# Kernel tuning notes

Measured on AMD Instinct MI355X. Metric: run time of the kernel, lower is better.

The kernel has to match this reference:

```python
import jax, jax.numpy as jnp
import numpy as np

N = 50000          # number of points
C = 64             # num_clusters (embedding width)
K_RAD = 32         # radius graph max_num_neighbors
K_KNN = 10         # knn graph k


def setup_inputs() -> dict:
    key = jax.random.key(0)
    ks = jax.random.split(key, 8)
    x0 = jax.random.normal(ks[0], (N, 3), jnp.float32)
    pos0 = jax.random.normal(ks[1], (N, 3), jnp.float32)
    # R0/t0 come from rigid_fitting in the original (external helper); use
    # orthonormal matrices from batched QR as realistic per-point rotations.
    A = jax.random.normal(ks[2], (N, 3, 3), jnp.float32)
    R0, _ = jnp.linalg.qr(A)
    t0 = jax.random.normal(ks[3], (N, 3), jnp.float32) * 0.1
    # pool1 k=1 assignment: point i -> cluster assign01[i]
    assign01 = jax.random.randint(ks[4], (N,), 0, C, dtype=jnp.int32)
    # radius graph edges (source, target): each point has K_RAD neighbors
    radius_src = jax.random.randint(ks[5], (N * K_RAD,), 0, N, dtype=jnp.int32)
    radius_dst = jnp.repeat(jnp.arange(N, dtype=jnp.int32), K_RAD)
    # knn-10 graph edges used by WeightedAvg
    knn_src = jax.random.randint(ks[6], (N * K_KNN,), 0, N, dtype=jnp.int32)
    knn_dst = jnp.repeat(jnp.arange(N, dtype=jnp.int32), K_KNN)
    return dict(x0=x0, pos0=pos0, R0=R0, t0=t0, assign01=assign01,
                radius_src=radius_src, radius_dst=radius_dst,
                knn_src=knn_src, knn_dst=knn_dst)


def _rigid_layer(xfeat, pos0, x0, R0, t0, src, dst):
    # RigidPropModule.message + max aggregation (nn=None, lin1: w=-1, b=0.01)
    Ri = R0[dst]                     # [E,3,3] target-side rotation
    ti = t0[dst]                     # [E,3]
    posj = pos0[src]                 # [E,3]
    xj = x0[src]                     # [E,3]
    pred = jnp.einsum('eij,ej->ei', Ri, posj) + ti
    d = jnp.sum((pred - xj) ** 2, axis=-1, keepdims=True)   # [E,1]
    w = jax.nn.sigmoid(-d + 0.01)
    msg = w * xfeat[src]             # [E,C]
    agg = jax.ops.segment_max(msg, dst, num_segments=xfeat.shape[0])
    # messages are non-negative; nodes with no edges get 0 (torch_scatter fill)
    return jnp.maximum(agg, 0.0)


def reference(x0, pos0, R0, t0, assign01, radius_src, radius_dst, knn_src, knn_dst):
    n = x0.shape[0]
    # scatter_add of one-hot cluster embeddings back to points
    emb = jnp.zeros((n, C), jnp.float32).at[jnp.arange(n), assign01].add(1.0)
    m1 = _rigid_layer(emb, pos0, x0, R0, t0, radius_src, radius_dst)
    m2 = _rigid_layer(m1, pos0, x0, R0, t0, radius_src, radius_dst)
    m3 = _rigid_layer(m2, pos0, x0, R0, t0, radius_src, radius_dst)
    m4 = _rigid_layer(m2, pos0, x0, R0, t0, radius_src, radius_dst)
    m5 = _rigid_layer(m2, pos0, x0, R0, t0, radius_src, radius_dst)
    msg = jnp.stack([m1.sum(-1), m2.sum(-1), m3.sum(-1),
                     m4.sum(-1), m5.sum(-1)], axis=-1)      # [N,5]
    # predictor: Linear(5,1) with w=ones, b=-17, then sigmoid
    conf = jax.nn.sigmoid(msg.sum(-1, keepdims=True) - 17.0)  # [N,1]
    # WeightedAvg over knn edges: out[t] = sum_s conf[s]*val[s] / sum_s conf[s]
    cw = conf[knn_src]                                       # [E,1]
    num_R = jax.ops.segment_sum(cw * R0.reshape(n, 9)[knn_src], knn_dst, num_segments=n)
    num_t = jax.ops.segment_sum(cw * t0[knn_src], knn_dst, num_segments=n)
    den = jax.ops.segment_sum(cw, knn_dst, num_segments=n) + 1e-8
    R_out = (num_R / den).reshape(n, 3, 3)
    t_out = num_t / den
    x_out = jnp.einsum('nij,nj->ni', R_out, pos0) + t_out
    return x_out, R_out, t_out
```

## Files before the change

kernel.cpp:

```cpp
#include <hip/hip_runtime.h>
#include <hip/hip_fp16.h>
#include <math.h>

#define N_PTS 50000
#define C_DIM 64
#define K_RAD 32
#define K_KNN 10

typedef unsigned int uv4 __attribute__((ext_vector_type(4)));
typedef unsigned int uv2 __attribute__((ext_vector_type(2)));

__device__ inline __half2 hmax2(__half2 a, __half2 b) {
    __half2 d;
    asm("v_pk_max_f16 %0, %1, %2" : "=v"(d) : "v"(a), "v"(b));
    return d;
}

__device__ inline __half2 shfl_xor_h2(__half2 v, int mask) {
    int i = *(int*)&v;
    int r = __shfl_xor(i, mask);
    return *(__half2*)&r;
}

__global__ void pack_tables_kernel(const float* __restrict__ pos0,
                                   const float* __restrict__ x0,
                                   const int* __restrict__ assign,
                                   float4* __restrict__ geo) {
    int i = blockIdx.x * blockDim.x + threadIdx.x;
    if (i >= N_PTS) return;
    geo[i * 2 + 0] = make_float4(pos0[3 * i], pos0[3 * i + 1], pos0[3 * i + 2], x0[3 * i]);
    geo[i * 2 + 1] = make_float4(x0[3 * i + 1], x0[3 * i + 2], __int_as_float(assign[i]), 0.0f);
}

__global__ void ew_layer1_kernel(const float4* __restrict__ geo,
                                 const float* __restrict__ R0,
                                 const float* __restrict__ t0,
                                 const int* __restrict__ src,
                                 unsigned int* __restrict__ packed,
                                 __half* __restrict__ m1,
                                 float4* __restrict__ rt4) {
    __shared__ int lm[16][C_DIM];
    __shared__ float ldsR[16 * 9];
    __shared__ float ldsT[16 * 3];
    float* rt4f = (float*)rt4;
    int tid = threadIdx.x;
    int blk = blockIdx.x;
    ((int*)lm)[tid] = 0;
    ((int*)lm)[tid + 256] = 0;
    ((int*)lm)[tid + 512] = 0;
    ((int*)lm)[tid + 768] = 0;
    if (tid < 144) ldsR[tid] = R0[blk * 144 + tid];
    if (tid < 48) ldsT[tid] = t0[blk * 48 + tid];
    int nl = tid >> 4;
    int ng = blk * 16 + nl;
    int e0 = tid & 15, e1 = e0 + 16;
    int s0 = __builtin_nontemporal_load(src + ng * K_RAD + e0);
    int s1 = __builtin_nontemporal_load(src + ng * K_RAD + e1);
    float4 g0a = geo[s0 * 2 + 0];
    float4 g0b = geo[s0 * 2 + 1];
    float4 g1a = geo[s1 * 2 + 0];
    float4 g1b = geo[s1 * 2 + 1];
    __syncthreads();
    if (tid < 48) {
        int n = tid / 3, slot = tid % 3;
        const float* Rp = ldsR + n * 9;
        const float* Tp = ldsT + n * 3;
        float4 q;
        if (slot == 0) q = make_float4(Rp[0], Rp[1], Rp[2], Rp[3]);
        else if (slot == 1) q = make_float4(Rp[4], Rp[5], Rp[6], Rp[7]);
        else q = make_float4(Rp[8], Tp[0], Tp[1], Tp[2]);
        rt4[(blk * 16 + n) * 4 + slot] = q;
    }
    const float* R = ldsR + nl * 9;
    const float* T = ldsT + nl * 3;
    float r0 = R[0] * g0a.x + R[1] * g0a.y + R[2] * g0a.z + T[0] - g0a.w;
    float r1 = R[3] * g0a.x + R[4] * g0a.y + R[5] * g0a.z + T[1] - g0b.x;
    float r2 = R[6] * g0a.x + R[7] * g0a.y + R[8] * g0a.z + T[2] - g0b.y;
    float d0 = r0 * r0 + r1 * r1 + r2 * r2;
    float w0 = 1.0f / (1.0f + __expf(d0 - 0.01f));
    float u0 = R[0] * g1a.x + R[1] * g1a.y + R[2] * g1a.z + T[0] - g1a.w;
    float u1 = R[3] * g1a.x + R[4] * g1a.y + R[5] * g1a.z + T[1] - g1b.x;
    float u2 = R[6] * g1a.x + R[7] * g1a.y + R[8] * g1a.z + T[2] - g1b.y;
    float d1 = u0 * u0 + u1 * u1 + u2 * u2;
    float w1 = 1.0f / (1.0f + __expf(d1 - 0.01f));
    unsigned int p0 =
        ((unsigned int)s0 << 16) | (unsigned int)__half_as_ushort(__float2half_rn(w0));
    unsigned int p1 =
        ((unsigned int)s1 << 16) | (unsigned int)__half_as_ushort(__float2half_rn(w1));
    __builtin_nontemporal_store(p0, packed + ng * K_RAD + e0);
    __builtin_nontemporal_store(p1, packed + ng * K_RAD + e1);
    atomicMax(&lm[nl][__float_as_int(g0b.z)], __float_as_int(w0));
    atomicMax(&lm[nl][__float_as_int(g1b.z)], __float_as_int(w1));
    __syncthreads();
    int c0 = (tid & 15) * 4;
    float v0 = __int_as_float(lm[nl][c0 + 0]);
    float v1 = __int_as_float(lm[nl][c0 + 1]);
    float v2 = __int_as_float(lm[nl][c0 + 2]);
    float v3 = __int_as_float(lm[nl][c0 + 3]);
    __half2 h01 = __floats2half2_rn(v0, v1);
    __half2 h23 = __floats2half2_rn(v2, v3);
    uint2 uo = make_uint2(*(unsigned int*)&h01, *(unsigned int*)&h23);
    *(uint2*)(m1 + ng * C_DIM + c0) = uo;
    float s = v0 + v1 + v2 + v3;
    s += __shfl_down(s, 8);
    s += __shfl_down(s, 4);
    s += __shfl_down(s, 2);
    s += __shfl_down(s, 1);
    if ((tid & 15) == 0) rt4f[ng * 16 + 12] = s - 17.0f;
}

__global__ void layer2_kernel(const unsigned int* __restrict__ packed,
                              const __half* __restrict__ xin,
                              __half* __restrict__ xout,
                              float* __restrict__ rt4f) {
    int gid = blockIdx.x * blockDim.x + threadIdx.x;
    int lane = gid & 63;
    int node = (gid >> 6) * 2 + (lane >> 5);
    int eslot = (lane >> 3) & 3;
    int cpos = lane & 7;
    const uv4* pk4 = (const uv4*)(packed + node * K_RAD + eslot * 8);
    uv4 q0 = __builtin_nontemporal_load(pk4);
    uv4 q1 = __builtin_nontemporal_load(pk4 + 1);
    unsigned int pes[8] = {q0.x, q0.y, q0.z, q0.w, q1.x, q1.y, q1.z, q1.w};
    float4 f[8];
#pragma unroll
    for (int p = 0; p < 8; ++p)
        f[p] = *(const float4*)(xin + (pes[p] >> 16) * C_DIM + cpos * 8);
    __half2 a0 = __float2half2_rn(0.0f), a1 = a0, a2 = a0, a3 = a0;
#pragma unroll
    for (int p = 0; p < 8; ++p) {
        __half2* h = (__half2*)&f[p];
        __half2 w2 = __half2half2(__ushort_as_half((unsigned short)(pes[p] & 0xffffu)));
        a0 = hmax2(a0, __hmul2(w2, h[0]));
        a1 = hmax2(a1, __hmul2(w2, h[1]));
        a2 = hmax2(a2, __hmul2(w2, h[2]));
        a3 = hmax2(a3, __hmul2(w2, h[3]));
    }
#pragma unroll
    for (int off = 8; off <= 16; off <<= 1) {
        a0 = hmax2(a0, shfl_xor_h2(a0, off));
        a1 = hmax2(a1, shfl_xor_h2(a1, off));
        a2 = hmax2(a2, shfl_xor_h2(a2, off));
        a3 = hmax2(a3, shfl_xor_h2(a3, off));
    }
    if (eslot == 0) {
        float4 o;
        __half2* oh = (__half2*)&o;
        oh[0] = a0; oh[1] = a1; oh[2] = a2; oh[3] = a3;
        ((float4*)(xout + node * C_DIM))[cpos] = o;
    }
    float2 v0 = __half22float2(a0), v1 = __half22float2(a1);
    float2 v2 = __half22float2(a2), v3 = __half22float2(a3);
    float s = v0.x + v0.y + v1.x + v1.y + v2.x + v2.y + v3.x + v3.y;
    s += __shfl_xor(s, 1);
    s += __shfl_xor(s, 2);
    s += __shfl_xor(s, 4);
    if ((lane & 31) == 0) rt4f[node * 16 + 13] = s;
}

__global__ void layer3_conf_kernel(const unsigned int* __restrict__ packed,
                                   const __half* __restrict__ xin,
                                   float* __restrict__ rt4f) {
    int gid = blockIdx.x * blockDim.x + threadIdx.x;
    int lane = gid & 63;
    int node = (gid >> 6) * 2 + (lane >> 5);
    int eslot = (lane >> 3) & 3;
    int cpos = lane & 7;
    const uv4* pk4 = (const uv4*)(packed + node * K_RAD + eslot * 8);
    uv4 q0 = __builtin_nontemporal_load(pk4);
    uv4 q1 = __builtin_nontemporal_load(pk4 + 1);
    unsigned int pes[8] = {q0.x, q0.y, q0.z, q0.w, q1.x, q1.y, q1.z, q1.w};
    float4 f[8];
#pragma unroll
    for (int p = 0; p < 8; ++p)
        f[p] = *(const float4*)(xin + (pes[p] >> 16) * C_DIM + cpos * 8);
    __half2 a0 = __float2half2_rn(0.0f), a1 = a0, a2 = a0, a3 = a0;
#pragma unroll
    for (int p = 0; p < 8; ++p) {
        __half2* h = (__half2*)&f[p];
        __half2 w2 = __half2half2(__ushort_as_half((unsigned short)(pes[p] & 0xffffu)));
        a0 = hmax2(a0, __hmul2(w2, h[0]));
        a1 = hmax2(a1, __hmul2(w2, h[1]));
        a2 = hmax2(a2, __hmul2(w2, h[2]));
        a3 = hmax2(a3, __hmul2(w2, h[3]));
    }
#pragma unroll
    for (int off = 8; off <= 16; off <<= 1) {
        a0 = hmax2(a0, shfl_xor_h2(a0, off));
        a1 = hmax2(a1, shfl_xor_h2(a1, off));
        a2 = hmax2(a2, shfl_xor_h2(a2, off));
        a3 = hmax2(a3, shfl_xor_h2(a3, off));
    }
    float2 v0 = __half22float2(a0), v1 = __half22float2(a1);
    float2 v2 = __half22float2(a2), v3 = __half22float2(a3);
    float s = v0.x + v0.y + v1.x + v1.y + v2.x + v2.y + v3.x + v3.y;
    s += __shfl_xor(s, 1);
    s += __shfl_xor(s, 2);
    s += __shfl_xor(s, 4);
    if ((lane & 31) == 0) {
        float base = rt4f[node * 16 + 12];
        float s2 = rt4f[node * 16 + 13];
        float tot = base + s2 + 3.0f * s;
        rt4f[node * 16 + 12] = 1.0f / (1.0f + __expf(-tot));
    }
}

__global__ void wavg_kernel(const int* __restrict__ knn_src,
                            const float4* __restrict__ rt4,
                            const float* __restrict__ pos0,
                            float* __restrict__ out) {
    int gid = blockIdx.x * blockDim.x + threadIdx.x;
    int lane = gid & 63;
    int t = gid >> 3;
    int part = lane & 3;
    int half = (lane >> 2) & 1;
    if (t >= N_PTS) return;
    int ids[5];
#pragma unroll
    for (int k = 0; k < 5; ++k)
        ids[k] = __builtin_nontemporal_load(knn_src + t * K_KNN + half * 5 + k);
    float4 q[5];
#pragma unroll
    for (int k = 0; k < 5; ++k) q[k] = rt4[ids[k] * 4 + part];
    float4 acc = make_float4(0.f, 0.f, 0.f, 0.f);
#pragma unroll
    for (int k = 0; k < 5; ++k) {
        float c = __shfl(q[k].x, lane | 3);
        if (part == 3) {
            acc.x += c;
        } else {
            acc.x += c * q[k].x; acc.y += c * q[k].y;
            acc.z += c * q[k].z; acc.w += c * q[k].w;
        }
    }
    acc.x += __shfl_xor(acc.x, 4);
    acc.y += __shfl_xor(acc.y, 4);
    acc.z += __shfl_xor(acc.z, 4);
    acc.w += __shfl_xor(acc.w, 4);
    float den = __shfl(acc.x, lane | 3) + 1e-8f;
    float inv = 1.0f / den;
    float4 sc = make_float4(acc.x * inv, acc.y * inv, acc.z * inv, acc.w * inv);
    int base = lane & ~3;
    float R3 = __shfl(sc.w, base + 0);
    float R6 = __shfl(sc.z, base + 1);
    float R7 = __shfl(sc.w, base + 1);
    float t0v = __shfl(sc.y, base + 2);
    float t1v = __shfl(sc.z, base + 2);
    if (half == 0) {
        float px = pos0[t * 3 + 0], py = pos0[t * 3 + 1], pz = pos0[t * 3 + 2];
        float* Rout = out + N_PTS * 3;
        float* tout = out + N_PTS * 12;
        if (part == 0) {
            __builtin_nontemporal_store(sc.x * px + sc.y * py + sc.z * pz + t0v, out + t * 3 + 0);
            __builtin_nontemporal_store(sc.x, Rout + t * 9 + 0);
            __builtin_nontemporal_store(sc.y, Rout + t * 9 + 1);
            __builtin_nontemporal_store(sc.z, Rout + t * 9 + 2);
            __builtin_nontemporal_store(sc.w, Rout + t * 9 + 3);
        } else if (part == 1) {
            __builtin_nontemporal_store(R3 * px + sc.x * py + sc.y * pz + t1v, out + t * 3 + 1);
            __builtin_nontemporal_store(sc.x, Rout + t * 9 + 4);
            __builtin_nontemporal_store(sc.y, Rout + t * 9 + 5);
            __builtin_nontemporal_store(sc.z, Rout + t * 9 + 6);
            __builtin_nontemporal_store(sc.w, Rout + t * 9 + 7);
        } else if (part == 2) {
            __builtin_nontemporal_store(R6 * px + R7 * py + sc.x * pz + sc.w, out + t * 3 + 2);
            __builtin_nontemporal_store(sc.x, Rout + t * 9 + 8);
            __builtin_nontemporal_store(sc.y, tout + t * 3 + 0);
            __builtin_nontemporal_store(sc.z, tout + t * 3 + 1);
            __builtin_nontemporal_store(sc.w, tout + t * 3 + 2);
        }
    }
}

extern "C" void kernel_launch(void* const* d_in, const int* in_sizes, int n_in,
                              void* d_out, int out_size, void* d_ws, size_t ws_size,
                              hipStream_t stream) {
    const float* x0 = (const float*)d_in[0];
    const float* pos0 = (const float*)d_in[1];
    const float* R0 = (const float*)d_in[2];
    const float* t0 = (const float*)d_in[3];
    const int* assign01 = (const int*)d_in[4];
    const int* radius_src = (const int*)d_in[5];
    const int* knn_src = (const int*)d_in[7];

    char* ws = (char*)d_ws;
    unsigned int* packed = (unsigned int*)ws;
    __half* mA = (__half*)(ws + 6400000);
    __half* mB = (__half*)(ws + 12800000);
    float4* geo = (float4*)(ws + 19200000);
    float4* rt4 = (float4*)(ws + 20800000);
    float* out = (float*)d_out;

    pack_tables_kernel<<<(N_PTS + 255) / 256, 256, 0, stream>>>(
        pos0, x0, assign01, geo);

    ew_layer1_kernel<<<N_PTS / 16, 256, 0, stream>>>(
        geo, R0, t0, radius_src, packed, mA, rt4);

    layer2_kernel<<<N_PTS / 8, 256, 0, stream>>>(
        packed, mA, mB, (float*)rt4);

    layer3_conf_kernel<<<N_PTS / 8, 256, 0, stream>>>(
        packed, mB, (float*)rt4);

    wavg_kernel<<<(N_PTS * 8 + 255) / 256, 256, 0, stream>>>(
        knn_src, rt4, pos0, out);
}
```

Measured before the change: 138.2 us.

## Map one wavefront per node in gather layers and drop nontemporal hints

The two gather-max layer kernels now assign a full 64-lane wavefront to each node instead of half a wavefront. Each lane gathers 4 neighbour rows instead of 8, and the cross-lane max reduction gains one more shuffle step. The grid doubles and launch bounds are added to allow higher occupancy and more memory-level parallelism. Separately, nontemporal load/store builtins are replaced with ordinary accesses throughout, which changes cache retention for the packed edge table that later kernels reread.

Measured after the change: 136.4 us, median of 2. No clear change (-1.3%).

```diff
diff --git a/kernel.cpp b/kernel.cpp
--- a/kernel.cpp
+++ b/kernel.cpp
@@ -8,7 +8,6 @@
 #define K_KNN 10
 
 typedef unsigned int uv4 __attribute__((ext_vector_type(4)));
-typedef unsigned int uv2 __attribute__((ext_vector_type(2)));
 
 __device__ inline __half2 hmax2(__half2 a, __half2 b) {
     __half2 d;
@@ -54,8 +53,8 @@
     int nl = tid >> 4;
     int ng = blk * 16 + nl;
     int e0 = tid & 15, e1 = e0 + 16;
-    int s0 = __builtin_nontemporal_load(src + ng * K_RAD + e0);
-    int s1 = __builtin_nontemporal_load(src + ng * K_RAD + e1);
+    int s0 = src[ng * K_RAD + e0];
+    int s1 = src[ng * K_RAD + e1];
     float4 g0a = geo[s0 * 2 + 0];
     float4 g0b = geo[s0 * 2 + 1];
     float4 g1a = geo[s1 * 2 + 0];
@@ -83,12 +82,10 @@
     float u2 = R[6] * g1a.x + R[7] * g1a.y + R[8] * g1a.z + T[2] - g1b.y;
     float d1 = u0 * u0 + u1 * u1 + u2 * u2;
     float w1 = 1.0f / (1.0f + __expf(d1 - 0.01f));
-    unsigned int p0 =
+    packed[ng * K_RAD + e0] =
         ((unsigned int)s0 << 16) | (unsigned int)__half_as_ushort(__float2half_rn(w0));
-    unsigned int p1 =
+    packed[ng * K_RAD + e1] =
         ((unsigned int)s1 << 16) | (unsigned int)__half_as_ushort(__float2half_rn(w1));
-    __builtin_nontemporal_store(p0, packed + ng * K_RAD + e0);
-    __builtin_nontemporal_store(p1, packed + ng * K_RAD + e1);
     atomicMax(&lm[nl][__float_as_int(g0b.z)], __float_as_int(w0));
     atomicMax(&lm[nl][__float_as_int(g1b.z)], __float_as_int(w1));
     __syncthreads();
@@ -109,26 +106,25 @@
     if ((tid & 15) == 0) rt4f[ng * 16 + 12] = s - 17.0f;
 }
 
-__global__ void layer2_kernel(const unsigned int* __restrict__ packed,
-                              const __half* __restrict__ xin,
-                              __half* __restrict__ xout,
-                              float* __restrict__ rt4f) {
+__global__ __launch_bounds__(256, 8)
+void layer2_kernel(const unsigned int* __restrict__ packed,
+                   const __half* __restrict__ xin,
+                   __half* __restrict__ xout,
+                   float* __restrict__ rt4f) {
     int gid = blockIdx.x * blockDim.x + threadIdx.x;
     int lane = gid & 63;
-    int node = (gid >> 6) * 2 + (lane >> 5);
-    int eslot = (lane >> 3) & 3;
+    int node = gid >> 6;
+    int eslot = lane >> 3;
     int cpos = lane & 7;
-    const uv4* pk4 = (const uv4*)(packed + node * K_RAD + eslot * 8);
-    uv4 q0 = __builtin_nontemporal_load(pk4);
-    uv4 q1 = __builtin_nontemporal_load(pk4 + 1);
-    unsigned int pes[8] = {q0.x, q0.y, q0.z, q0.w, q1.x, q1.y, q1.z, q1.w};
-    float4 f[8];
-#pragma unroll
-    for (int p = 0; p < 8; ++p)
+    uv4 pk = *(const uv4*)(packed + node * K_RAD + eslot * 4);
+    unsigned int pes[4] = {pk.x, pk.y, pk.z, pk.w};
+    float4 f[4];
+#pragma unroll
+    for (int p = 0; p < 4; ++p)
         f[p] = *(const float4*)(xin + (pes[p] >> 16) * C_DIM + cpos * 8);
     __half2 a0 = __float2half2_rn(0.0f), a1 = a0, a2 = a0, a3 = a0;
 #pragma unroll
-    for (int p = 0; p < 8; ++p) {
+    for (int p = 0; p < 4; ++p) {
         __half2* h = (__half2*)&f[p];
         __half2 w2 = __half2half2(__ushort_as_half((unsigned short)(pes[p] & 0xffffu)));
         a0 = hmax2(a0, __hmul2(w2, h[0]));
@@ -137,7 +133,7 @@
         a3 = hmax2(a3, __hmul2(w2, h[3]));
     }
 #pragma unroll
-    for (int off = 8; off <= 16; off <<= 1) {
+    for (int off = 8; off <= 32; off <<= 1) {
         a0 = hmax2(a0, shfl_xor_h2(a0, off));
         a1 = hmax2(a1, shfl_xor_h2(a1, off));
         a2 = hmax2(a2, shfl_xor_h2(a2, off));
@@ -155,28 +151,27 @@
     s += __shfl_xor(s, 1);
     s += __shfl_xor(s, 2);
     s += __shfl_xor(s, 4);
-    if ((lane & 31) == 0) rt4f[node * 16 + 13] = s;
-}
-
-__global__ void layer3_conf_kernel(const unsigned int* __restrict__ packed,
-                                   const __half* __restrict__ xin,
-                                   float* __restrict__ rt4f) {
+    if (lane == 0) rt4f[node * 16 + 13] = s;
+}
+
+__global__ __launch_bounds__(256, 8)
+void layer3_conf_kernel(const unsigned int* __restrict__ packed,
+                        const __half* __restrict__ xin,
+                        float* __restrict__ rt4f) {
     int gid = blockIdx.x * blockDim.x + threadIdx.x;
     int lane = gid & 63;
-    int node = (gid >> 6) * 2 + (lane >> 5);
-    int eslot = (lane >> 3) & 3;
+    int node = gid >> 6;
+    int eslot = lane >> 3;
     int cpos = lane & 7;
-    const uv4* pk4 = (const uv4*)(packed + node * K_RAD + eslot * 8);
-    uv4 q0 = __builtin_nontemporal_load(pk4);
-    uv4 q1 = __builtin_nontemporal_load(pk4 + 1);
-    unsigned int pes[8] = {q0.x, q0.y, q0.z, q0.w, q1.x, q1.y, q1.z, q1.w};
-    float4 f[8];
-#pragma unroll
-    for (int p = 0; p < 8; ++p)
+    uv4 pk = *(const uv4*)(packed + node * K_RAD + eslot * 4);
+    unsigned int pes[4] = {pk.x, pk.y, pk.z, pk.w};
+    float4 f[4];
+#pragma unroll
+    for (int p = 0; p < 4; ++p)
         f[p] = *(const float4*)(xin + (pes[p] >> 16) * C_DIM + cpos * 8);
     __half2 a0 = __float2half2_rn(0.0f), a1 = a0, a2 = a0, a3 = a0;
 #pragma unroll
-    for (int p = 0; p < 8; ++p) {
+    for (int p = 0; p < 4; ++p) {
         __half2* h = (__half2*)&f[p];
         __half2 w2 = __half2half2(__ushort_as_half((unsigned short)(pes[p] & 0xffffu)));
         a0 = hmax2(a0, __hmul2(w2, h[0]));
@@ -185,7 +180,7 @@
         a3 = hmax2(a3, __hmul2(w2, h[3]));
     }
 #pragma unroll
-    for (int off = 8; off <= 16; off <<= 1) {
+    for (int off = 8; off <= 32; off <<= 1) {
         a0 = hmax2(a0, shfl_xor_h2(a0, off));
         a1 = hmax2(a1, shfl_xor_h2(a1, off));
         a2 = hmax2(a2, shfl_xor_h2(a2, off));
@@ -197,7 +192,7 @@
     s += __shfl_xor(s, 1);
     s += __shfl_xor(s, 2);
     s += __shfl_xor(s, 4);
-    if ((lane & 31) == 0) {
+    if (lane == 0) {
         float base = rt4f[node * 16 + 12];
         float s2 = rt4f[node * 16 + 13];
         float tot = base + s2 + 3.0f * s;
@@ -217,8 +212,7 @@
     if (t >= N_PTS) return;
     int ids[5];
 #pragma unroll
-    for (int k = 0; k < 5; ++k)
-        ids[k] = __builtin_nontemporal_load(knn_src + t * K_KNN + half * 5 + k);
+    for (int k = 0; k < 5; ++k) ids[k] = knn_src[t * K_KNN + half * 5 + k];
     float4 q[5];
 #pragma unroll
     for (int k = 0; k < 5; ++k) q[k] = rt4[ids[k] * 4 + part];
@@ -251,23 +245,17 @@
         float* Rout = out + N_PTS * 3;
         float* tout = out + N_PTS * 12;
         if (part == 0) {
-            __builtin_nontemporal_store(sc.x * px + sc.y * py + sc.z * pz + t0v, out + t * 3 + 0);
-            __builtin_nontemporal_store(sc.x, Rout + t * 9 + 0);
-            __builtin_nontemporal_store(sc.y, Rout + t * 9 + 1);
-            __builtin_nontemporal_store(sc.z, Rout + t * 9 + 2);
-            __builtin_nontemporal_store(sc.w, Rout + t * 9 + 3);
+            out[t * 3 + 0] = sc.x * px + sc.y * py + sc.z * pz + t0v;
+            Rout[t * 9 + 0] = sc.x; Rout[t * 9 + 1] = sc.y;
+            Rout[t * 9 + 2] = sc.z; Rout[t * 9 + 3] = sc.w;
         } else if (part == 1) {
-            __builtin_nontemporal_store(R3 * px + sc.x * py + sc.y * pz + t1v, out + t * 3 + 1);
-            __builtin_nontemporal_store(sc.x, Rout + t * 9 + 4);
-            __builtin_nontemporal_store(sc.y, Rout + t * 9 + 5);
-            __builtin_nontemporal_store(sc.z, Rout + t * 9 + 6);
-            __builtin_nontemporal_store(sc.w, Rout + t * 9 + 7);
+            out[t * 3 + 1] = R3 * px + sc.x * py + sc.y * pz + t1v;
+            Rout[t * 9 + 4] = sc.x; Rout[t * 9 + 5] = sc.y;
+            Rout[t * 9 + 6] = sc.z; Rout[t * 9 + 7] = sc.w;
         } else if (part == 2) {
-            __builtin_nontemporal_store(R6 * px + R7 * py + sc.x * pz + sc.w, out + t * 3 + 2);
-            __builtin_nontemporal_store(sc.x, Rout + t * 9 + 8);
-            __builtin_nontemporal_store(sc.y, tout + t * 3 + 0);
-            __builtin_nontemporal_store(sc.z, tout + t * 3 + 1);
-            __builtin_nontemporal_store(sc.w, tout + t * 3 + 2);
+            out[t * 3 + 2] = R6 * px + R7 * py + sc.x * pz + sc.w;
+            Rout[t * 9 + 8] = sc.x;
+            tout[t * 3 + 0] = sc.y; tout[t * 3 + 1] = sc.z; tout[t * 3 + 2] = sc.w;
         }
     }
 }
@@ -297,10 +285,10 @@
     ew_layer1_kernel<<<N_PTS / 16, 256, 0, stream>>>(
         geo, R0, t0, radius_src, packed, mA, rt4);
 
-    layer2_kernel<<<N_PTS / 8, 256, 0, stream>>>(
+    layer2_kernel<<<N_PTS / 4, 256, 0, stream>>>(
         packed, mA, mB, (float*)rt4);
 
-    layer3_conf_kernel<<<N_PTS / 8, 256, 0, stream>>>(
+    layer3_conf_kernel<<<N_PTS / 4, 256, 0, stream>>>(
         packed, mB, (float*)rt4);
 
     wavg_kernel<<<(N_PTS * 8 + 255) / 256, 256, 0, stream>>>(
```
